# Kernel tuning notes

Hardware: AMD Instinct MI355X
Metric: run time of the kernel (lower is better)

Reference implementation:

```python
import jax, jax.numpy as jnp
import numpy as np

N_NODES = 100000
N_EDGES = 2000000
IN_C = 64
OUT_C = 64
K = 27
G = 4


def setup_inputs() -> dict:
    key = jax.random.key(0)
    k1, k2, k3, k4, k5, k6 = jax.random.split(key, 6)
    inp = {
        "input": jax.random.normal(k1, (N_NODES, IN_C), dtype=jnp.float32),
        "i": jax.random.randint(k2, (N_EDGES,), 0, N_NODES),
        "j": jax.random.randint(k3, (N_EDGES,), 0, N_NODES),
        "k": jax.random.randint(k4, (N_EDGES,), 0, K),
        "n": N_NODES,
        "weight": jax.random.normal(k5, (IN_C, OUT_C // G, K), dtype=jnp.float32) * 0.1,
        "bias": jax.random.normal(k6, (OUT_C,), dtype=jnp.float32) * 0.1,
    }
    return inp


def reference(input, i, j, k, n, weight, bias):
    # weight: [in_c, out_c//g, K] -> w: [K, g, in_c//g, out_c//g]
    w = weight.reshape(G, IN_C // G, OUT_C // G, K).transpose(3, 0, 1, 2)
    x3 = input.reshape(input.shape[0], G, IN_C // G)  # [n, g, c]
    # Transform every node by every kernel-position weight once (n*K small GEMMs)
    # instead of materializing a per-edge [E,g,c,d] weight gather.
    x_all = jnp.einsum('ngc,kgcd->nkgd', x3, w)  # [n, K, g, d]
    msgs = x_all[j, k]                            # [E, g, d] gather per edge
    out = jax.ops.segment_sum(msgs, i, num_segments=n)  # scatter-add to dst nodes
    out = out.reshape(-1, OUT_C) + bias
    return out
```

## Files before the change

### kernel.cpp

```cpp
#include <hip/hip_runtime.h>
#include <hip/hip_bf16.h>


#define KPOS 27
#define WPACK_UINTS (KPOS * 512)
#define SCAN_NB 256

typedef unsigned u32x4 __attribute__((ext_vector_type(4)));

__device__ __forceinline__ unsigned packbf(float a, float b) {
    unsigned ua = (unsigned)__bfloat16_as_ushort(__float2bfloat16(a));
    unsigned ub = (unsigned)__bfloat16_as_ushort(__float2bfloat16(b));
    return ua | (ub << 16);
}

#define DOT2(A, X, W) asm("v_dot2_f32_bf16 %0, %1, %2, %0" : "+v"(A) : "v"(X), "v"(W))

#define GLOAD(DST, VOFF, BASE) \
    asm volatile("global_load_dwordx4 %0, %1, %2" : "=v"(DST) : "v"(VOFF), "s"(BASE))
#define GLOAD16(DST, VOFF, BASE) \
    asm volatile("global_load_dwordx4 %0, %1, %2 offset:16" : "=v"(DST) : "v"(VOFF), "s"(BASE))

__global__ void init_out_kernel(float* __restrict__ out, const float* __restrict__ bias, int total) {
    int idx = blockIdx.x * blockDim.x + threadIdx.x;
    if (idx < total) out[idx] = bias[idx & 63];
}
__global__ void edge_kernel_rawW(const float* __restrict__ input, const int* __restrict__ ei,
                                 const int* __restrict__ ej, const int* __restrict__ ek,
                                 const float* __restrict__ weight, float* __restrict__ out, int n_edges) {
    const int lane = threadIdx.x & 63;
    const int g16 = lane & 48;
    const int d = lane & 15;
    int wave = (blockIdx.x * blockDim.x + threadIdx.x) >> 6;
    int n_waves = (gridDim.x * blockDim.x) >> 6;
    for (int e = wave; e < n_edges; e += n_waves) {
        int ie = ei[e], je = ej[e], ke = ek[e];
        float x = input[je * 64 + lane];
        float acc = 0.0f;
        #pragma unroll
        for (int c = 0; c < 16; ++c)
            acc += __shfl(x, g16 + c, 64) * weight[(g16 + c) * 432 + d * 27 + ke];
        atomicAdd(out + ie * 64 + lane, acc);
    }
}

__global__ void prep_kernel(const float* __restrict__ input, const float* __restrict__ weight,
                            unsigned* __restrict__ xb, unsigned* __restrict__ wp,
                            int* __restrict__ cnt, int n_nodes, int nquads) {
    int t = blockIdx.x * blockDim.x + threadIdx.x;
    if (t < n_nodes) cnt[t] = 0;
    if (t < WPACK_UINTS) {
        int k  = t >> 9;
        int r  = t & 511;
        int q  = r >> 8;
        int r2 = r & 255;
        int gc = r2 >> 2;
        int m  = r2 & 3;
        int g = gc >> 4, d = gc & 15;
        int c = (q * 4 + m) * 2;
        int ic = g * 16 + c;
        float f0 = weight[ic * 432 + d * 27 + k];
        float f1 = weight[(ic + 1) * 432 + d * 27 + k];
        wp[t] = packbf(f0, f1);
    }
    if (t < nquads) {
        const float4* in4 = (const float4*)input;
        float4 a = in4[2 * t], b = in4[2 * t + 1];
        uint4 o;
        o.x = packbf(a.x, a.y);
        o.y = packbf(a.z, a.w);
        o.z = packbf(b.x, b.y);
        o.w = packbf(b.z, b.w);
        ((uint4*)xb)[t] = o;
    }
}

__global__ void rank_kernel(const int* __restrict__ ei, int* __restrict__ cnt,
                            unsigned short* __restrict__ rank, int n_edges) {
    int e = blockIdx.x * blockDim.x + threadIdx.x;
    if (e < n_edges)
        rank[e] = (unsigned short)atomicAdd(&cnt[ei[e]], 1);
}

__global__ void scanA_kernel(const int* __restrict__ cnt, int* __restrict__ partial,
                             int n, int chunk) {
    __shared__ int red[256];
    int b = blockIdx.x;
    int lo = b * chunk, hi = min(lo + chunk, n);
    int s = 0;
    for (int v = lo + threadIdx.x; v < hi; v += 256) s += cnt[v];
    red[threadIdx.x] = s;
    __syncthreads();
    for (int d = 128; d > 0; d >>= 1) {
        if (threadIdx.x < d) red[threadIdx.x] += red[threadIdx.x + d];
        __syncthreads();
    }
    if (threadIdx.x == 0) partial[b] = red[0];
}

__global__ void scanB_kernel(int* __restrict__ partial, int* __restrict__ off, int n) {
    __shared__ int sums[SCAN_NB];
    int t = threadIdx.x;
    sums[t] = partial[t];
    __syncthreads();
    for (int d = 1; d < SCAN_NB; d <<= 1) {
        int val = (t >= d) ? sums[t - d] : 0;
        __syncthreads();
        sums[t] += val;
        __syncthreads();
    }
    partial[t] = (t == 0) ? 0 : sums[t - 1];
    if (t == SCAN_NB - 1) off[n] = sums[t];
}

__global__ void scanC_kernel(const int* __restrict__ cnt, const int* __restrict__ partial,
                             int* __restrict__ off, int n, int chunk) {
    __shared__ int excl[256];
    int b = blockIdx.x;
    int lo = b * chunk, hi = min(lo + chunk, n);
    int per = (chunk + 255) >> 8;
    int tlo = lo + threadIdx.x * per;
    int thi = min(tlo + per, hi);
    int s = 0;
    for (int v = tlo; v < thi; ++v) s += cnt[v];
    excl[threadIdx.x] = s;
    __syncthreads();
    for (int d = 1; d < 256; d <<= 1) {
        int val = (threadIdx.x >= d) ? excl[threadIdx.x - d] : 0;
        __syncthreads();
        excl[threadIdx.x] += val;
        __syncthreads();
    }
    int run = partial[b] + ((threadIdx.x == 0) ? 0 : excl[threadIdx.x - 1]);
    for (int v = tlo; v < thi; ++v) { off[v] = run; run += cnt[v]; }
}

__global__ void fill_kernel(const int* __restrict__ ei, const int* __restrict__ ej,
                            const int* __restrict__ ek, const int* __restrict__ off,
                            const unsigned short* __restrict__ rank,
                            unsigned* __restrict__ jk, int n_edges) {
    int e = blockIdx.x * blockDim.x + threadIdx.x;
    if (e < n_edges)
        jk[off[ei[e]] + (int)rank[e]] = (unsigned)ej[e] | ((unsigned)ek[e] << 17);
}

__launch_bounds__(1024, 8)
__global__ void gather_kernel(const unsigned* __restrict__ xb,
                              const unsigned* __restrict__ jk,
                              const int* __restrict__ off,
                              const unsigned* __restrict__ wp,
                              const float* __restrict__ bias,
                              float* __restrict__ out, int n) {
    __shared__ unsigned lds[WPACK_UINTS];
    for (int t = threadIdx.x; t < WPACK_UINTS / 4; t += blockDim.x)
        ((uint4*)lds)[t] = ((const uint4*)wp)[t];
    __syncthreads();

    const int lane = threadIdx.x & 63;
    const unsigned gby = (unsigned)((lane & 48) << 1);
    const float b  = bias[lane];
    const unsigned* wl = lds + (lane << 2);

    int wid = (blockIdx.x * blockDim.x + threadIdx.x) >> 6;
    int nw  = (gridDim.x * blockDim.x) >> 6;

    for (int v = wid; v < n; v += nw) {
        int e0 = off[v];
        int e1 = off[v + 1];
        float a0l = 0.0f, a0h = 0.0f, a1l = 0.0f, a1h = 0.0f;
        int e = e0;

        for (; e + 4 <= e1; e += 4) {
            unsigned p0 = jk[e], p1 = jk[e + 1], p2 = jk[e + 2], p3 = jk[e + 3];
            unsigned o0 = ((p0 & 0x1FFFFu) << 7) + gby;
            unsigned o1 = ((p1 & 0x1FFFFu) << 7) + gby;
            unsigned o2 = ((p2 & 0x1FFFFu) << 7) + gby;
            unsigned o3 = ((p3 & 0x1FFFFu) << 7) + gby;
            u32x4 xa0, xc0, xa1, xc1, xa2, xc2, xa3, xc3;
            GLOAD  (xa0, o0, xb);
            GLOAD16(xc0, o0, xb);
            GLOAD  (xa1, o1, xb);
            GLOAD16(xc1, o1, xb);
            GLOAD  (xa2, o2, xb);
            GLOAD16(xc2, o2, xb);
            GLOAD  (xa3, o3, xb);
            GLOAD16(xc3, o3, xb);
            asm volatile("s_waitcnt vmcnt(0)");
            __builtin_amdgcn_sched_barrier(0);
            {
                const u32x4* wr = (const u32x4*)(wl + ((p0 >> 17) << 9));
                u32x4 wa = wr[0], wb = wr[64];
                DOT2(a0l, xa0[0], wa[0]); DOT2(a0h, xa0[1], wa[1]);
                DOT2(a0l, xa0[2], wa[2]); DOT2(a0h, xa0[3], wa[3]);
                DOT2(a0l, xc0[0], wb[0]); DOT2(a0h, xc0[1], wb[1]);
                DOT2(a0l, xc0[2], wb[2]); DOT2(a0h, xc0[3], wb[3]);
            }
            {
                const u32x4* wr = (const u32x4*)(wl + ((p1 >> 17) << 9));
                u32x4 wa = wr[0], wb = wr[64];
                DOT2(a1l, xa1[0], wa[0]); DOT2(a1h, xa1[1], wa[1]);
                DOT2(a1l, xa1[2], wa[2]); DOT2(a1h, xa1[3], wa[3]);
                DOT2(a1l, xc1[0], wb[0]); DOT2(a1h, xc1[1], wb[1]);
                DOT2(a1l, xc1[2], wb[2]); DOT2(a1h, xc1[3], wb[3]);
            }
            {
                const u32x4* wr = (const u32x4*)(wl + ((p2 >> 17) << 9));
                u32x4 wa = wr[0], wb = wr[64];
                DOT2(a0l, xa2[0], wa[0]); DOT2(a0h, xa2[1], wa[1]);
                DOT2(a0l, xa2[2], wa[2]); DOT2(a0h, xa2[3], wa[3]);
                DOT2(a0l, xc2[0], wb[0]); DOT2(a0h, xc2[1], wb[1]);
                DOT2(a0l, xc2[2], wb[2]); DOT2(a0h, xc2[3], wb[3]);
            }
            {
                const u32x4* wr = (const u32x4*)(wl + ((p3 >> 17) << 9));
                u32x4 wa = wr[0], wb = wr[64];
                DOT2(a1l, xa3[0], wa[0]); DOT2(a1h, xa3[1], wa[1]);
                DOT2(a1l, xa3[2], wa[2]); DOT2(a1h, xa3[3], wa[3]);
                DOT2(a1l, xc3[0], wb[0]); DOT2(a1h, xc3[1], wb[1]);
                DOT2(a1l, xc3[2], wb[2]); DOT2(a1h, xc3[3], wb[3]);
            }
        }

#define EDGE_BODY(P, AL, AH)                                                \
        do {                                                                \
            unsigned p_ = (P);                                              \
            const u32x4* wr = (const u32x4*)(wl + ((p_ >> 17) << 9));       \
            const u32x4* xr = (const u32x4*)(xb + ((p_ & 0x1FFFFu) << 5) + (gby >> 2)); \
            u32x4 xa = xr[0], xc = xr[1];                                   \
            u32x4 wa = wr[0], wb = wr[64];                                  \
            DOT2(AL, xa[0], wa[0]); DOT2(AH, xa[1], wa[1]);                 \
            DOT2(AL, xa[2], wa[2]); DOT2(AH, xa[3], wa[3]);                 \
            DOT2(AL, xc[0], wb[0]); DOT2(AH, xc[1], wb[1]);                 \
            DOT2(AL, xc[2], wb[2]); DOT2(AH, xc[3], wb[3]);                 \
        } while (0)

        for (; e + 2 <= e1; e += 2) {
            unsigned p0 = jk[e], p1 = jk[e + 1];
            EDGE_BODY(p0, a0l, a0h);
            EDGE_BODY(p1, a1l, a1h);
        }
        if (e < e1) EDGE_BODY(jk[e], a0l, a0h);
#undef EDGE_BODY

        out[(v << 6) + lane] = (a0l + a0h) + (a1l + a1h) + b;
    }
}

static inline size_t al256(size_t x) { return (x + 255) & ~(size_t)255; }

extern "C" void kernel_launch(void* const* d_in, const int* in_sizes, int n_in,
                              void* d_out, int out_size, void* d_ws, size_t ws_size,
                              hipStream_t stream) {
    const float* input  = (const float*)d_in[0];
    const int*   ei     = (const int*)d_in[1];
    const int*   ej     = (const int*)d_in[2];
    const int*   ek     = (const int*)d_in[3];
    const float* weight = (const float*)d_in[5];
    const float* bias   = (const float*)d_in[6];

    const int n_edges = in_sizes[1];
    const int n_nodes = out_size / 64;

    size_t off_o  = 0;
    size_t off_s  = al256((size_t)(n_nodes + 1) * 4);
    size_t cnt_o  = off_o + off_s;
    size_t cnt_s  = al256((size_t)n_nodes * 4);
    size_t par_o  = cnt_o + cnt_s;
    size_t par_s  = al256((size_t)SCAN_NB * 4);
    size_t rank_o = par_o + par_s;
    size_t rank_s = al256((size_t)n_edges * 2);
    size_t jk_o   = rank_o + rank_s;
    size_t jk_s   = al256((size_t)n_edges * 4);
    size_t wp_o   = jk_o + jk_s;
    size_t wp_s   = al256((size_t)WPACK_UINTS * 4);
    size_t xb_o   = wp_o + wp_s;
    size_t xb_s   = al256((size_t)n_nodes * 64 * 2);
    size_t need   = xb_o + xb_s;

    if (ws_size < need) {
        int blocks = (out_size + 255) / 256;
        hipLaunchKernelGGL(init_out_kernel, dim3(blocks), dim3(256), 0, stream,
                           (float*)d_out, bias, out_size);
        hipLaunchKernelGGL(edge_kernel_rawW, dim3(2048), dim3(256), 0, stream,
                           input, ei, ej, ek, weight, (float*)d_out, n_edges);
        return;
    }

    char* ws = (char*)d_ws;
    int*            off  = (int*)(ws + off_o);
    int*            cnt  = (int*)(ws + cnt_o);
    int*            par  = (int*)(ws + par_o);
    unsigned short* rank = (unsigned short*)(ws + rank_o);
    unsigned*       jk   = (unsigned*)(ws + jk_o);
    unsigned*       wp   = (unsigned*)(ws + wp_o);
    unsigned*       xb   = (unsigned*)(ws + xb_o);

    const int eb = (n_edges + 255) / 256;
    const int nquads = n_nodes * 8;
    const int prep_range = max(nquads, max(n_nodes, WPACK_UINTS));
    const int chunk = (n_nodes + SCAN_NB - 1) / SCAN_NB;

    hipLaunchKernelGGL(prep_kernel, dim3((prep_range + 255) / 256), dim3(256), 0, stream,
                       input, weight, xb, wp, cnt, n_nodes, nquads);
    hipLaunchKernelGGL(rank_kernel, dim3(eb), dim3(256), 0, stream, ei, cnt, rank, n_edges);
    hipLaunchKernelGGL(scanA_kernel, dim3(SCAN_NB), dim3(256), 0, stream, cnt, par, n_nodes, chunk);
    hipLaunchKernelGGL(scanB_kernel, dim3(1), dim3(SCAN_NB), 0, stream, par, off, n_nodes);
    hipLaunchKernelGGL(scanC_kernel, dim3(SCAN_NB), dim3(256), 0, stream, cnt, par, off, n_nodes, chunk);
    hipLaunchKernelGGL(fill_kernel, dim3(eb), dim3(256), 0, stream, ei, ej, ek, off, rank, jk, n_edges);

    hipLaunchKernelGGL(gather_kernel, dim3(512), dim3(1024), 0, stream,
                       xb, jk, off, wp, bias, (float*)d_out, n_nodes);
}
```

Baseline: 304.1 us.

## Switch gather to edge-balanced partitioning with run-length atomic flushes

The gather kernel now splits the sorted edge list evenly across waves instead of assigning whole destination nodes per wave. Each record stores the destination id alongside the packed source/kernel index. A wave accumulates until the destination changes, then flushes with an atomicAdd. Output is bias-initialized in the prep kernel. This targets load imbalance from uneven node degrees, at the cost of doubled record traffic, atomics at segment boundaries, and dropping the explicit batched inline-asm loads with vmcnt wait.

```diff
diff --git a/kernel.cpp b/kernel.cpp
--- a/kernel.cpp
+++ b/kernel.cpp
@@ -15,11 +15,6 @@
 }
 
 #define DOT2(A, X, W) asm("v_dot2_f32_bf16 %0, %1, %2, %0" : "+v"(A) : "v"(X), "v"(W))
-
-#define GLOAD(DST, VOFF, BASE) \
-    asm volatile("global_load_dwordx4 %0, %1, %2" : "=v"(DST) : "v"(VOFF), "s"(BASE))
-#define GLOAD16(DST, VOFF, BASE) \
-    asm volatile("global_load_dwordx4 %0, %1, %2 offset:16" : "=v"(DST) : "v"(VOFF), "s"(BASE))
 
 __global__ void init_out_kernel(float* __restrict__ out, const float* __restrict__ bias, int total) {
     int idx = blockIdx.x * blockDim.x + threadIdx.x;
@@ -45,8 +40,9 @@
 }
 
 __global__ void prep_kernel(const float* __restrict__ input, const float* __restrict__ weight,
+                            const float* __restrict__ bias, float* __restrict__ out,
                             unsigned* __restrict__ xb, unsigned* __restrict__ wp,
-                            int* __restrict__ cnt, int n_nodes, int nquads) {
+                            int* __restrict__ cnt, int n_nodes, int nquads, int nout4) {
     int t = blockIdx.x * blockDim.x + threadIdx.x;
     if (t < n_nodes) cnt[t] = 0;
     if (t < WPACK_UINTS) {
@@ -73,6 +69,9 @@
         o.w = packbf(b.z, b.w);
         ((uint4*)xb)[t] = o;
     }
+    if (t < nout4) {
+        ((float4*)out)[t] = ((const float4*)bias)[t & 15];
+    }
 }
 
 __global__ void rank_kernel(const int* __restrict__ ei, int* __restrict__ cnt,
@@ -138,94 +137,54 @@
 __global__ void fill_kernel(const int* __restrict__ ei, const int* __restrict__ ej,
                             const int* __restrict__ ek, const int* __restrict__ off,
                             const unsigned short* __restrict__ rank,
-                            unsigned* __restrict__ jk, int n_edges) {
+                            uint2* __restrict__ recs, int n_edges) {
     int e = blockIdx.x * blockDim.x + threadIdx.x;
-    if (e < n_edges)
-        jk[off[ei[e]] + (int)rank[e]] = (unsigned)ej[e] | ((unsigned)ek[e] << 17);
+    if (e < n_edges) {
+        int ie = ei[e];
+        uint2 r;
+        r.x = (unsigned)ej[e] | ((unsigned)ek[e] << 17);
+        r.y = (unsigned)ie;
+        recs[off[ie] + (int)rank[e]] = r;
+    }
 }
 
 __launch_bounds__(1024, 8)
 __global__ void gather_kernel(const unsigned* __restrict__ xb,
-                              const unsigned* __restrict__ jk,
-                              const int* __restrict__ off,
+                              const uint2* __restrict__ recs,
                               const unsigned* __restrict__ wp,
-                              const float* __restrict__ bias,
-                              float* __restrict__ out, int n) {
+                              float* __restrict__ out, int n_edges) {
     __shared__ unsigned lds[WPACK_UINTS];
     for (int t = threadIdx.x; t < WPACK_UINTS / 4; t += blockDim.x)
         ((uint4*)lds)[t] = ((const uint4*)wp)[t];
     __syncthreads();
 
     const int lane = threadIdx.x & 63;
-    const unsigned gby = (unsigned)((lane & 48) << 1);
-    const float b  = bias[lane];
+    const int g8   = (lane & 48) >> 1;
     const unsigned* wl = lds + (lane << 2);
 
     int wid = (blockIdx.x * blockDim.x + threadIdx.x) >> 6;
     int nw  = (gridDim.x * blockDim.x) >> 6;
-
-    for (int v = wid; v < n; v += nw) {
-        int e0 = off[v];
-        int e1 = off[v + 1];
-        float a0l = 0.0f, a0h = 0.0f, a1l = 0.0f, a1h = 0.0f;
-        int e = e0;
-
-        for (; e + 4 <= e1; e += 4) {
-            unsigned p0 = jk[e], p1 = jk[e + 1], p2 = jk[e + 2], p3 = jk[e + 3];
-            unsigned o0 = ((p0 & 0x1FFFFu) << 7) + gby;
-            unsigned o1 = ((p1 & 0x1FFFFu) << 7) + gby;
-            unsigned o2 = ((p2 & 0x1FFFFu) << 7) + gby;
-            unsigned o3 = ((p3 & 0x1FFFFu) << 7) + gby;
-            u32x4 xa0, xc0, xa1, xc1, xa2, xc2, xa3, xc3;
-            GLOAD  (xa0, o0, xb);
-            GLOAD16(xc0, o0, xb);
-            GLOAD  (xa1, o1, xb);
-            GLOAD16(xc1, o1, xb);
-            GLOAD  (xa2, o2, xb);
-            GLOAD16(xc2, o2, xb);
-            GLOAD  (xa3, o3, xb);
-            GLOAD16(xc3, o3, xb);
-            asm volatile("s_waitcnt vmcnt(0)");
-            __builtin_amdgcn_sched_barrier(0);
-            {
-                const u32x4* wr = (const u32x4*)(wl + ((p0 >> 17) << 9));
-                u32x4 wa = wr[0], wb = wr[64];
-                DOT2(a0l, xa0[0], wa[0]); DOT2(a0h, xa0[1], wa[1]);
-                DOT2(a0l, xa0[2], wa[2]); DOT2(a0h, xa0[3], wa[3]);
-                DOT2(a0l, xc0[0], wb[0]); DOT2(a0h, xc0[1], wb[1]);
-                DOT2(a0l, xc0[2], wb[2]); DOT2(a0h, xc0[3], wb[3]);
-            }
-            {
-                const u32x4* wr = (const u32x4*)(wl + ((p1 >> 17) << 9));
-                u32x4 wa = wr[0], wb = wr[64];
-                DOT2(a1l, xa1[0], wa[0]); DOT2(a1h, xa1[1], wa[1]);
-                DOT2(a1l, xa1[2], wa[2]); DOT2(a1h, xa1[3], wa[3]);
-                DOT2(a1l, xc1[0], wb[0]); DOT2(a1h, xc1[1], wb[1]);
-                DOT2(a1l, xc1[2], wb[2]); DOT2(a1h, xc1[3], wb[3]);
-            }
-            {
-                const u32x4* wr = (const u32x4*)(wl + ((p2 >> 17) << 9));
-                u32x4 wa = wr[0], wb = wr[64];
-                DOT2(a0l, xa2[0], wa[0]); DOT2(a0h, xa2[1], wa[1]);
-                DOT2(a0l, xa2[2], wa[2]); DOT2(a0h, xa2[3], wa[3]);
-                DOT2(a0l, xc2[0], wb[0]); DOT2(a0h, xc2[1], wb[1]);
-                DOT2(a0l, xc2[2], wb[2]); DOT2(a0h, xc2[3], wb[3]);
-            }
-            {
-                const u32x4* wr = (const u32x4*)(wl + ((p3 >> 17) << 9));
-                u32x4 wa = wr[0], wb = wr[64];
-                DOT2(a1l, xa3[0], wa[0]); DOT2(a1h, xa3[1], wa[1]);
-                DOT2(a1l, xa3[2], wa[2]); DOT2(a1h, xa3[3], wa[3]);
-                DOT2(a1l, xc3[0], wb[0]); DOT2(a1h, xc3[1], wb[1]);
-                DOT2(a1l, xc3[2], wb[2]); DOT2(a1h, xc3[3], wb[3]);
-            }
-        }
+    int epw = (((n_edges + nw - 1) / nw) + 7) & ~7;
+    int e    = wid * epw;
+    int eend = min(e + epw, n_edges);
+    if (e >= eend) return;
+
+    int  cur = -1;
+    float a0l = 0.0f, a0h = 0.0f, a1l = 0.0f, a1h = 0.0f;
+
+#define FLUSH_CHANGE() do {                                                   \
+        if (cur >= 0) {                                                       \
+            float s_ = (a0l + a0h) + (a1l + a1h);                             \
+            atomicAdd(out + (cur << 6) + lane, s_);                           \
+            a0l = a0h = a1l = a1h = 0.0f;                                     \
+        }                                                                     \
+    } while (0)
 
 #define EDGE_BODY(P, AL, AH)                                                \
         do {                                                                \
             unsigned p_ = (P);                                              \
             const u32x4* wr = (const u32x4*)(wl + ((p_ >> 17) << 9));       \
-            const u32x4* xr = (const u32x4*)(xb + ((p_ & 0x1FFFFu) << 5) + (gby >> 2)); \
+            const u32x4* xr = (const u32x4*)(xb + ((p_ & 0x1FFFFu) << 5) + g8); \
             u32x4 xa = xr[0], xc = xr[1];                                   \
             u32x4 wa = wr[0], wb = wr[64];                                  \
             DOT2(AL, xa[0], wa[0]); DOT2(AH, xa[1], wa[1]);                 \
@@ -234,16 +193,70 @@
             DOT2(AL, xc[2], wb[2]); DOT2(AH, xc[3], wb[3]);                 \
         } while (0)
 
-        for (; e + 2 <= e1; e += 2) {
-            unsigned p0 = jk[e], p1 = jk[e + 1];
-            EDGE_BODY(p0, a0l, a0h);
-            EDGE_BODY(p1, a1l, a1h);
+    for (; e + 4 <= eend; e += 4) {
+        const uint4* rc = (const uint4*)(recs + e);
+        uint4 r01 = rc[0], r23 = rc[1];
+        const u32x4* x0 = (const u32x4*)(xb + ((r01.x & 0x1FFFFu) << 5) + g8);
+        const u32x4* x1 = (const u32x4*)(xb + ((r01.z & 0x1FFFFu) << 5) + g8);
+        const u32x4* x2 = (const u32x4*)(xb + ((r23.x & 0x1FFFFu) << 5) + g8);
+        const u32x4* x3 = (const u32x4*)(xb + ((r23.z & 0x1FFFFu) << 5) + g8);
+        u32x4 xa0 = x0[0], xc0 = x0[1];
+        u32x4 xa1 = x1[0], xc1 = x1[1];
+        u32x4 xa2 = x2[0], xc2 = x2[1];
+        u32x4 xa3 = x3[0], xc3 = x3[1];
+        int i0 = __builtin_amdgcn_readfirstlane((int)r01.y);
+        int i1 = __builtin_amdgcn_readfirstlane((int)r01.w);
+        int i2 = __builtin_amdgcn_readfirstlane((int)r23.y);
+        int i3 = __builtin_amdgcn_readfirstlane((int)r23.w);
+
+        if (i0 != cur) { FLUSH_CHANGE(); cur = i0; }
+        {
+            const u32x4* wr = (const u32x4*)(wl + ((r01.x >> 17) << 9));
+            u32x4 wa = wr[0], wb2 = wr[64];
+            DOT2(a0l, xa0[0], wa[0]); DOT2(a0h, xa0[1], wa[1]);
+            DOT2(a0l, xa0[2], wa[2]); DOT2(a0h, xa0[3], wa[3]);
+            DOT2(a0l, xc0[0], wb2[0]); DOT2(a0h, xc0[1], wb2[1]);
+            DOT2(a0l, xc0[2], wb2[2]); DOT2(a0h, xc0[3], wb2[3]);
         }
-        if (e < e1) EDGE_BODY(jk[e], a0l, a0h);
+        if (i1 != cur) { FLUSH_CHANGE(); cur = i1; }
+        {
+            const u32x4* wr = (const u32x4*)(wl + ((r01.z >> 17) << 9));
+            u32x4 wa = wr[0], wb2 = wr[64];
+            DOT2(a1l, xa1[0], wa[0]); DOT2(a1h, xa1[1], wa[1]);
+            DOT2(a1l, xa1[2], wa[2]); DOT2(a1h, xa1[3], wa[3]);
+            DOT2(a1l, xc1[0], wb2[0]); DOT2(a1h, xc1[1], wb2[1]);
+            DOT2(a1l, xc1[2], wb2[2]); DOT2(a1h, xc1[3], wb2[3]);
+        }
+        if (i2 != cur) { FLUSH_CHANGE(); cur = i2; }
+        {
+            const u32x4* wr = (const u32x4*)(wl + ((r23.x >> 17) << 9));
+            u32x4 wa = wr[0], wb2 = wr[64];
+            DOT2(a0l, xa2[0], wa[0]); DOT2(a0h, xa2[1], wa[1]);
+            DOT2(a0l, xa2[2], wa[2]); DOT2(a0h, xa2[3], wa[3]);
+            DOT2(a0l, xc2[0], wb2[0]); DOT2(a0h, xc2[1], wb2[1]);
+            DOT2(a0l, xc2[2], wb2[2]); DOT2(a0h, xc2[3], wb2[3]);
+        }
+        if (i3 != cur) { FLUSH_CHANGE(); cur = i3; }
+        {
+            const u32x4* wr = (const u32x4*)(wl + ((r23.z >> 17) << 9));
+            u32x4 wa = wr[0], wb2 = wr[64];
+            DOT2(a1l, xa3[0], wa[0]); DOT2(a1h, xa3[1], wa[1]);
+            DOT2(a1l, xa3[2], wa[2]); DOT2(a1h, xa3[3], wa[3]);
+            DOT2(a1l, xc3[0], wb2[0]); DOT2(a1h, xc3[1], wb2[1]);
+            DOT2(a1l, xc3[2], wb2[2]); DOT2(a1h, xc3[3], wb2[3]);
+        }
+    }
+
+    for (; e < eend; ++e) {
+        uint2 r = recs[e];
+        int ri = __builtin_amdgcn_readfirstlane((int)r.y);
+        if (ri != cur) { FLUSH_CHANGE(); cur = ri; }
+        EDGE_BODY(r.x, a0l, a0h);
+    }
+
+    FLUSH_CHANGE();
 #undef EDGE_BODY
-
-        out[(v << 6) + lane] = (a0l + a0h) + (a1l + a1h) + b;
-    }
+#undef FLUSH_CHANGE
 }
 
 static inline size_t al256(size_t x) { return (x + 255) & ~(size_t)255; }
@@ -269,9 +282,9 @@
     size_t par_s  = al256((size_t)SCAN_NB * 4);
     size_t rank_o = par_o + par_s;
     size_t rank_s = al256((size_t)n_edges * 2);
-    size_t jk_o   = rank_o + rank_s;
-    size_t jk_s   = al256((size_t)n_edges * 4);
-    size_t wp_o   = jk_o + jk_s;
+    size_t rec_o  = rank_o + rank_s;
+    size_t rec_s  = al256((size_t)n_edges * 8);
+    size_t wp_o   = rec_o + rec_s;
     size_t wp_s   = al256((size_t)WPACK_UINTS * 4);
     size_t xb_o   = wp_o + wp_s;
     size_t xb_s   = al256((size_t)n_nodes * 64 * 2);
@@ -291,23 +304,25 @@
     int*            cnt  = (int*)(ws + cnt_o);
     int*            par  = (int*)(ws + par_o);
     unsigned short* rank = (unsigned short*)(ws + rank_o);
-    unsigned*       jk   = (unsigned*)(ws + jk_o);
+    uint2*          recs = (uint2*)(ws + rec_o);
     unsigned*       wp   = (unsigned*)(ws + wp_o);
     unsigned*       xb   = (unsigned*)(ws + xb_o);
 
     const int eb = (n_edges + 255) / 256;
     const int nquads = n_nodes * 8;
-    const int prep_range = max(nquads, max(n_nodes, WPACK_UINTS));
+    const int nout4  = n_nodes * 16;
+    const int prep_range = max(max(nquads, nout4), max(n_nodes, WPACK_UINTS));
     const int chunk = (n_nodes + SCAN_NB - 1) / SCAN_NB;
 
     hipLaunchKernelGGL(prep_kernel, dim3((prep_range + 255) / 256), dim3(256), 0, stream,
-                       input, weight, xb, wp, cnt, n_nodes, nquads);
+                       input, weight, bias, (float*)d_out, xb, wp, cnt,
+                       n_nodes, nquads, nout4);
     hipLaunchKernelGGL(rank_kernel, dim3(eb), dim3(256), 0, stream, ei, cnt, rank, n_edges);
     hipLaunchKernelGGL(scanA_kernel, dim3(SCAN_NB), dim3(256), 0, stream, cnt, par, n_nodes, chunk);
     hipLaunchKernelGGL(scanB_kernel, dim3(1), dim3(SCAN_NB), 0, stream, par, off, n_nodes);
     hipLaunchKernelGGL(scanC_kernel, dim3(SCAN_NB), dim3(256), 0, stream, cnt, par, off, n_nodes, chunk);
-    hipLaunchKernelGGL(fill_kernel, dim3(eb), dim3(256), 0, stream, ei, ej, ek, off, rank, jk, n_edges);
+    hipLaunchKernelGGL(fill_kernel, dim3(eb), dim3(256), 0, stream, ei, ej, ek, off, rank, recs, n_edges);
 
     hipLaunchKernelGGL(gather_kernel, dim3(512), dim3(1024), 0, stream,
-                       xb, jk, off, wp, bias, (float*)d_out, n_nodes);
-}
+                       xb, recs, wp, (float*)d_out, n_edges);
+}
```

Measured after the change: 299.7 us. No clear change (-1.4%).
